# Kernel tuning notes

Measured on AMD Instinct MI355X. Metric: run time of the kernel, lower is better.

Reference implementation:

```python
import jax, jax.numpy as jnp
import numpy as np

B, L, WD, H = 16, 48, 1024, 1024
RANK_H = 128
TEMP = 1.0


def setup_inputs():
    key = jax.random.key(0)
    ks = jax.random.split(key, 10)
    se = jax.random.normal(ks[0], (B, L, WD), jnp.float32)
    length = jnp.clip(jax.random.randint(ks[1], (B,), 8, L + 1), 2, L)
    gumbel_u = jax.random.uniform(ks[2], (B, L), jnp.float32, minval=1e-6, maxval=1.0 - 1e-6)
    sc = 0.02
    Wih = jax.random.normal(ks[3], (4 * H, WD), jnp.float32) * sc
    Whh = jax.random.normal(ks[4], (4 * H, H), jnp.float32) * sc
    bih = jnp.zeros((4 * H,), jnp.float32).at[H:2 * H].set(1.0)  # forget-gate bias = 1
    bhh = jnp.zeros((4 * H,), jnp.float32)
    R1 = jax.random.normal(ks[5], (RANK_H, H), jnp.float32) * 0.01  # rank Linear 1 (no bias)
    R2 = jax.random.normal(ks[6], (1, RANK_H), jnp.float32) * 0.01  # rank Linear 2 (no bias)
    Wc = jax.random.normal(ks[7], (6 * H, 3 * H), jnp.float32) * sc  # Nary compose linear
    bc = jnp.zeros((6 * H,), jnp.float32)
    return dict(sentence_embedding=se, gumbel_u=gumbel_u, Wih=Wih, Whh=Whh,
                bih=bih, bhh=bhh, R1=R1, R2=R2, Wc=Wc, bc=bc, length=length)


def leaf_lstm(x, Wih, Whh, bih, bhh):
    # torch.nn.LSTMCell over time; x: [B, L, WD] -> hs, cs: [B, L, H]
    h0 = jnp.zeros((x.shape[0], H), x.dtype)

    def step(carry, xt):
        h, c = carry
        g = xt @ Wih.T + bih + h @ Whh.T + bhh
        i, f, u, o = jnp.split(g, 4, axis=-1)  # torch gate order i, f, g, o
        c = jax.nn.sigmoid(f) * c + jax.nn.sigmoid(i) * jnp.tanh(u)
        h = jax.nn.sigmoid(o) * jnp.tanh(c)
        return (h, c), (h, c)

    _, (hs, cs) = jax.lax.scan(step, (h0, h0), jnp.swapaxes(x, 0, 1))
    return jnp.swapaxes(hs, 0, 1), jnp.swapaxes(cs, 0, 1)


def nary_cell(lh, lc, rh, rc, xh, xc, Wc, bc):
    # 3-ary tree-LSTM composition: gates i, f_left, f_right, f_x, u, o
    g = jnp.concatenate([lh, rh, xh], axis=-1) @ Wc.T + bc
    i, fl, fr, fx, u, o = jnp.split(g, 6, axis=-1)
    c = (jax.nn.sigmoid(i) * jnp.tanh(u) + jax.nn.sigmoid(fl) * lc
         + jax.nn.sigmoid(fr) * rc + jax.nn.sigmoid(fx) * xc)
    h = jax.nn.sigmoid(o) * jnp.tanh(c)
    return h, c


def build(hs, cs, noise, start, end, R1, R2, Wc, bc):
    # hs, cs: [L, H] for one sentence; returns (h, c) each [H]
    if end <= start:
        z = jnp.zeros((H,), hs.dtype)
        return z, z
    if end == start + 1:
        return hs[start], cs[start]
    x = jax.lax.stop_gradient(hs[start:end])          # rank_detach=True
    s = (jax.nn.relu(x @ R1.T) @ R2.T)[:, 0]          # rank MLP scores [n]
    pos = start + int(jnp.argmax(s))                  # split point = noiseless argmax
    soft = jax.nn.softmax((s + noise[start:end]) / TEMP)
    hard = jax.nn.one_hot(int(jnp.argmax(soft)), end - start, dtype=soft.dtype)
    gate = soft + jax.lax.stop_gradient(hard - soft)  # straight-through gumbel-softmax
    h = gate @ hs[start:end]
    c = gate @ cs[start:end]
    lh, lc = build(hs, cs, noise, start, pos, R1, R2, Wc, bc)
    rh, rc = build(hs, cs, noise, pos + 1, end, R1, R2, Wc, bc)
    return nary_cell(lh, lc, rh, rc, h, c, Wc, bc)


def reference(sentence_embedding, gumbel_u, Wih, Whh, bih, bhh, R1, R2, Wc, bc, length):
    noise = -jnp.log(-jnp.log(gumbel_u))  # Gumbel(0, 1) noise
    hs, cs = leaf_lstm(sentence_embedding, Wih, Whh, bih, bhh)
    lens = [int(v) for v in np.asarray(length)]
    h_res, c_res = [], []
    for b in range(B):
        h, c = build(hs[b], cs[b], noise[b], 0, lens[b], R1, R2, Wc, bc)
        h_res.append(h)
        c_res.append(c)
    return jnp.stack([jnp.stack(h_res), jnp.stack(c_res)])  # [2, B, H]
```

## Files before the change

### kernel.cpp

```cpp
#include <hip/hip_runtime.h>
#include <math.h>

#define BB 16
#define LL 48
#define HH 1024
#define NG4 4096
#define NG6 6144
#define K3H 3072
#define RANKH 128
#define MAXN 47
#define TOTN (BB*MAXN)
#define MAXLVL 48
#define MAXNPL 384

#define FSTRIDE 32
#define FDOM 8192
#define HS_S 1028

typedef __attribute__((ext_vector_type(8))) short bf16x8;
typedef __attribute__((ext_vector_type(4))) float f32x4;

__device__ __forceinline__ float sigf(float x){ return 1.f/(1.f + expf(-x)); }

__device__ __forceinline__ unsigned short f2bf(float f){
  union { float f; unsigned u; } v; v.f = f;
  unsigned r = v.u + 0x7fff + ((v.u >> 16) & 1);
  return (unsigned short)(r >> 16);
}

__device__ __forceinline__ void st_llc(float* p, float v){
  __hip_atomic_store(p, v, __ATOMIC_RELAXED, __HIP_MEMORY_SCOPE_AGENT);
}
__device__ __forceinline__ float ld_llc(const float* p){
  return __hip_atomic_load(p, __ATOMIC_RELAXED, __HIP_MEMORY_SCOPE_AGENT);
}
__device__ __forceinline__ void st_llc_u16(unsigned short* p, unsigned v){
  asm volatile("global_store_short %0, %1, off sc0 sc1" :: "v"(p), "v"(v) : "memory");
}
__device__ __forceinline__ void st_llc_u32(unsigned* p, unsigned v){
  asm volatile("global_store_dword %0, %1, off sc0 sc1" :: "v"(p), "v"(v) : "memory");
}
__device__ __forceinline__ void wait_vm0(){
  asm volatile("s_waitcnt vmcnt(0)" ::: "memory");
}

__device__ __forceinline__ void flagbar(unsigned* flags, unsigned p, int* ldsok){
  wait_vm0();
  __syncthreads();
  int tid = threadIdx.x;
  if (tid == 0)
    st_llc_u32(&flags[blockIdx.x*FSTRIDE], p);
  for (;;){
    unsigned v;
    asm volatile("global_load_dword %0, %1, off sc0 sc1"
                 : "=v"(v) : "v"(&flags[tid*FSTRIDE]));
    wait_vm0();
    int all64 = __all((int)(v >= p));
    if ((tid & 63) == 0) ldsok[tid >> 6] = all64;
    __syncthreads();
    if (ldsok[0] & ldsok[1] & ldsok[2] & ldsok[3]) break;
    __builtin_amdgcn_s_sleep(1);
    __syncthreads();
  }
}

__global__ __launch_bounds__(256) void k_init(unsigned* flags, unsigned short* zrow){
  int tid = threadIdx.x;
  for (int i = tid; i < 2*FDOM; i += 256) flags[i] = 0u;
  for (int i = tid; i < 1024; i += 256) zrow[i] = 0;
}

__global__ __launch_bounds__(256) void k_cvt_bf16(const float* __restrict__ in,
    unsigned short* __restrict__ out, int n){
  int i = (blockIdx.x*256 + threadIdx.x)*4;
  if (i >= n) return;
  float4 v = *(const float4*)(in + i);
  ushort4 o;
  o.x = f2bf(v.x); o.y = f2bf(v.y); o.z = f2bf(v.z); o.w = f2bf(v.w);
  *(ushort4*)(out + i) = o;
}

__global__ __launch_bounds__(256) void k_transpose(const float* __restrict__ in,
                                                   float* __restrict__ out, int R, int C){
  __shared__ float t[32][33];
  int bx = blockIdx.x*32, by = blockIdx.y*32;
  int x = threadIdx.x, y = threadIdx.y;
  #pragma unroll
  for (int i = 0; i < 32; i += 8){
    int r = by + y + i, c = bx + x;
    if (r < R && c < C) t[y+i][x] = in[(size_t)r*C + c];
  }
  __syncthreads();
  #pragma unroll
  for (int i = 0; i < 32; i += 8){
    int r = bx + y + i, c = by + x;
    if (r < C && c < R) out[(size_t)r*R + c] = t[x][y+i];
  }
}

__global__ __launch_bounds__(256) void k_gemm_gx(const float* __restrict__ A,
    const float* __restrict__ Bw, const float* __restrict__ bih,
    const float* __restrict__ bhh, float* __restrict__ Cout, int M, int N, int K){
  __shared__ float as[16][68];
  __shared__ float bs[16][68];
  int m0 = blockIdx.x*64, n0 = blockIdx.y*64;
  int tid = threadIdx.x;
  int mt = tid & 15, nt = tid >> 4;
  float acc[4][4] = {};
  for (int k0 = 0; k0 < K; k0 += 16){
    #pragma unroll
    for (int it = 0; it < 4; ++it){
      int idx = it*256 + tid;
      int kk = idx & 15, mm = idx >> 4;
      as[kk][mm] = A[(size_t)(m0+mm)*K + k0 + kk];
      bs[kk][mm] = Bw[(size_t)(n0+mm)*K + k0 + kk];
    }
    __syncthreads();
    #pragma unroll
    for (int kk = 0; kk < 16; ++kk){
      float a4[4], b4[4];
      #pragma unroll
      for (int i = 0; i < 4; ++i) a4[i] = as[kk][mt*4+i];
      #pragma unroll
      for (int i = 0; i < 4; ++i) b4[i] = bs[kk][nt*4+i];
      #pragma unroll
      for (int i = 0; i < 4; ++i)
        #pragma unroll
        for (int j2 = 0; j2 < 4; ++j2) acc[i][j2] += a4[i]*b4[j2];
    }
    __syncthreads();
  }
  #pragma unroll
  for (int i = 0; i < 4; ++i){
    int m = m0 + mt*4 + i;
    #pragma unroll
    for (int j2 = 0; j2 < 4; ++j2){
      int n = n0 + nt*4 + j2;
      Cout[(size_t)m*N + n] = acc[i][j2] + bih[n] + bhh[n];
    }
  }
}

__global__ __launch_bounds__(256) void k_gx_t(const float* __restrict__ Gx,
                                              float* __restrict__ Gxt){
  __shared__ float t2[16][257];
  int t = blockIdx.x;
  int rc = blockIdx.y;
  int tid = threadIdx.x;
  #pragma unroll
  for (int m = 0; m < 16; ++m)
    t2[m][tid] = Gx[((size_t)(m*48 + t))*4096 + rc*256 + tid];
  __syncthreads();
  int rl = tid >> 4, m = tid & 15;
  #pragma unroll
  for (int i = 0; i < 16; ++i){
    int r = rc*256 + i*16 + rl;
    Gxt[((size_t)t*4096 + r)*16 + m] = t2[m][i*16 + rl];
  }
}

__global__ __launch_bounds__(256, 1) void k_lstm_scan(
    const float* __restrict__ Whh, const float* __restrict__ Gxt,
    float* __restrict__ hx,
    float* __restrict__ hs, float* __restrict__ cs,
    unsigned short* __restrict__ hs_bf, unsigned* __restrict__ flags){
  __shared__ float smem[17408];
  __shared__ float gbuf[4*64];
  __shared__ float cbuf[64];
  __shared__ int ldsok[4];
  int tid = threadIdx.x;
  int g = tid >> 6, kc = tid & 63;
  int j0 = blockIdx.x * 4;
  float w[4][16];
  #pragma unroll
  for (int jj = 0; jj < 4; ++jj){
    const float* src = Whh + (size_t)(g*1024 + j0 + jj)*1024 + kc*4;
    #pragma unroll
    for (int r = 0; r < 4; ++r){
      float4 v = *(const float4*)(src + r*256);
      w[jj][r*4+0]=v.x; w[jj][r*4+1]=v.y; w[jj][r*4+2]=v.z; w[jj][r*4+3]=v.w;
    }
  }
  if (tid < 64) cbuf[tid] = 0.f;
  for (int t = 0; t < LL; ++t){
    float gx = Gxt[((size_t)t*NG4 + g*1024 + j0 + (kc & 3))*16 + (kc >> 2)];
    float G = 0.f;
    if (t > 0){
      const float* slab = hx + (size_t)(t-1)*16384;
      f32x4 hv[16];
      #pragma unroll
      for (int i = 0; i < 16; ++i)
        hv[i] = *(const f32x4*)(slab + i*1024 + tid*4);
      {
        int mb = (tid & 3) * 4;
        int jb = tid >> 2;
        #pragma unroll
        for (int i = 0; i < 16; ++i){
          #pragma unroll
          for (int e = 0; e < 4; ++e)
            smem[(size_t)(mb + e)*HS_S + i*64 + jb] = hv[i][e];
        }
      }
      __syncthreads();
      float acc[4][16];
      #pragma unroll 4
      for (int m = 0; m < 16; ++m){
        const float* hb = &smem[(size_t)m*HS_S + (kc<<2)];
        float4 h0 = *(const float4*)(hb);
        float4 h1 = *(const float4*)(hb+256);
        float4 h2 = *(const float4*)(hb+512);
        float4 h3 = *(const float4*)(hb+768);
        #pragma unroll
        for (int jj = 0; jj < 4; ++jj){
          float s = w[jj][0]*h0.x + w[jj][1]*h0.y + w[jj][2]*h0.z + w[jj][3]*h0.w
                  + w[jj][4]*h1.x + w[jj][5]*h1.y + w[jj][6]*h1.z + w[jj][7]*h1.w
                  + w[jj][8]*h2.x + w[jj][9]*h2.y + w[jj][10]*h2.z + w[jj][11]*h2.w
                  + w[jj][12]*h3.x + w[jj][13]*h3.y + w[jj][14]*h3.z + w[jj][15]*h3.w;
          acc[jj][m] = s;
        }
      }
      __syncthreads();
      #pragma unroll
      for (int m = 0; m < 16; ++m){
        float4 v;
        v.x = acc[0][m]; v.y = acc[1][m]; v.z = acc[2][m]; v.w = acc[3][m];
        *(float4*)&smem[(size_t)(g*64 + kc)*68 + m*4] = v;
      }
      __syncthreads();
      {
        float s0=0.f,s1=0.f,s2=0.f,s3=0.f;
        #pragma unroll 4
        for (int l = 0; l < 64; l += 4){
          s0 += smem[(size_t)(g*64 + l  )*68 + kc];
          s1 += smem[(size_t)(g*64 + l+1)*68 + kc];
          s2 += smem[(size_t)(g*64 + l+2)*68 + kc];
          s3 += smem[(size_t)(g*64 + l+3)*68 + kc];
        }
        G = (s0+s1)+(s2+s3);
      }
    }
    gbuf[g*64 + kc] = G + gx;
    __syncthreads();
    if (g == 0){
      int o = kc;
      int jj = o >> 4, m = o & 15;
      int op = m*4 + jj;
      float gi = gbuf[0*64 + op];
      float gf = gbuf[1*64 + op];
      float gu = gbuf[2*64 + op];
      float go = gbuf[3*64 + op];
      float cp = cbuf[op];
      float c = sigf(gf)*cp + sigf(gi)*tanhf(gu);
      float h = sigf(go)*tanhf(c);
      cbuf[op] = c;
      st_llc(&hx[(size_t)t*16384 + j0*16 + o], h);
      size_t oidx = ((size_t)(m*LL + t))*HH + j0 + jj;
      hs[oidx] = h;
      cs[oidx] = c;
      hs_bf[oidx] = f2bf(h);
    }
    if (t < LL-1)
      flagbar(flags, (unsigned)(t+1), ldsok);
  }
}

__global__ __launch_bounds__(128) void k_score(const float* __restrict__ R1t,
    const float* __restrict__ R2, const float* __restrict__ hs,
    const float* __restrict__ gumbel_u, float* __restrict__ score,
    float* __restrict__ snoisy){
  __shared__ float hsm[HH];
  __shared__ float red[128];
  int bt = blockIdx.x;
  int tid = threadIdx.x;
  for (int i = tid; i < HH; i += 128) hsm[i] = hs[(size_t)bt*HH + i];
  __syncthreads();
  float acc = 0.f;
  for (int k = 0; k < HH; ++k) acc += R1t[(size_t)k*RANKH + tid] * hsm[k];
  red[tid] = fmaxf(acc, 0.f) * R2[tid];
  __syncthreads();
  for (int s = 64; s > 0; s >>= 1){
    if (tid < s) red[tid] += red[tid+s];
    __syncthreads();
  }
  if (tid == 0){
    float s = red[0];
    float u = gumbel_u[bt];
    float noise = -logf(-logf(u));
    score[bt]  = s;
    snoisy[bt] = s + noise;
  }
}

__global__ __launch_bounds__(64) void k_build(const float* __restrict__ score,
    const float* __restrict__ snoisy, const int* __restrict__ length,
    int* __restrict__ node_l, int* __restrict__ node_r, int* __restrict__ node_x,
    int* __restrict__ node_lvl, int* __restrict__ node_b, int* __restrict__ node_root,
    int* __restrict__ level_count, int* __restrict__ level_off, int* __restrict__ order){
  __shared__ float sc[BB*LL], sn[BB*LL];
  __shared__ int lcount[MAXLVL+1], lcur[MAXLVL+1], loff[MAXLVL+1];
  __shared__ int percnt[BB];
  int tid = threadIdx.x;
  for (int i = tid; i < BB*LL; i += 64){ sc[i] = score[i]; sn[i] = snoisy[i]; }
  for (int i = tid; i <= MAXLVL; i += 64){ lcount[i] = 0; lcur[i] = 0; }
  __syncthreads();
  if (tid < BB){
    int b = tid;
    int len = length[b];
    if (len > LL) len = LL;
    int qs[MAXN], qe[MAXN], qn[MAXN];
    int qh = 0, qt = 0, cnt = 0;
    int rootn = cnt++;
    qs[qt] = 0; qe[qt] = len; qn[qt] = rootn; qt++;
    while (qh < qt){
      int s0 = qs[qh], e0 = qe[qh], nid = qn[qh]; qh++;
      float best = sc[b*LL + s0]; int pos = s0;
      for (int t2 = s0+1; t2 < e0; ++t2){
        float v = sc[b*LL + t2];
        if (v > best){ best = v; pos = t2; }
      }
      float bestn = sn[b*LL + s0]; int js = s0;
      for (int t2 = s0+1; t2 < e0; ++t2){
        float v = sn[b*LL + t2];
        if (v > bestn){ bestn = v; js = t2; }
      }
      int gid = b*MAXN + nid;
      node_x[gid] = js;
      node_b[gid] = b;
      node_root[gid] = (nid == 0) ? 1 : 0;
      int ln = pos - s0, enc_l, enc_r;
      if (ln <= 0) enc_l = -1;
      else if (ln == 1) enc_l = 10000 + s0;
      else { int c2 = cnt++; enc_l = b*MAXN + c2; qs[qt]=s0; qe[qt]=pos; qn[qt]=c2; qt++; }
      int rn = e0 - (pos+1);
      if (rn <= 0) enc_r = -1;
      else if (rn == 1) enc_r = 10000 + (pos+1);
      else { int c2 = cnt++; enc_r = b*MAXN + c2; qs[qt]=pos+1; qe[qt]=e0; qn[qt]=c2; qt++; }
      node_l[gid] = enc_l; node_r[gid] = enc_r;
    }
    for (int i = cnt-1; i >= 0; --i){
      int gid = b*MAXN + i;
      int el = node_l[gid], er = node_r[gid];
      int llv = (el >= 0 && el < 10000) ? node_lvl[el] : 0;
      int rlv = (er >= 0 && er < 10000) ? node_lvl[er] : 0;
      node_lvl[gid] = 1 + (llv > rlv ? llv : rlv);
    }
    for (int i = 0; i < cnt; ++i) atomicAdd(&lcount[node_lvl[b*MAXN + i]], 1);
    percnt[b] = cnt;
  }
  __syncthreads();
  if (tid == 0){
    int off = 0, nlev = 0;
    for (int lv = 1; lv <= MAXLVL; ++lv){
      loff[lv] = off;
      level_off[lv] = off;
      level_count[lv] = lcount[lv];
      if (lcount[lv] > 0) nlev = lv;
      off += lcount[lv];
    }
    level_count[0] = nlev;
  }
  __syncthreads();
  if (tid < BB){
    int b = tid;
    int cnt = percnt[b];
    for (int i = 0; i < cnt; ++i){
      int gid = b*MAXN + i;
      int lv = node_lvl[gid];
      int p = atomicAdd(&lcur[lv], 1);
      order[loff[lv] + p] = gid;
    }
  }
}

__global__ __launch_bounds__(256, 1) void k_tree(
    const unsigned short* __restrict__ Wc_bf,
    const unsigned short* __restrict__ hs_bf,
    unsigned short* __restrict__ nodeH_bf,
    const unsigned short* __restrict__ zrow,
    const float* __restrict__ bc, const float* __restrict__ cs,
    float* __restrict__ nodeC,
    const int* __restrict__ node_l, const int* __restrict__ node_r,
    const int* __restrict__ node_x, const int* __restrict__ node_b,
    const int* __restrict__ node_root, const int* __restrict__ level_count,
    const int* __restrict__ level_off, const int* __restrict__ order,
    float* __restrict__ gates, float* __restrict__ out,
    unsigned* __restrict__ flags){
  __shared__ __align__(16) unsigned char wlds[24*6144];
  __shared__ int ldsok[4];
  int tid = threadIdx.x;
  int lane = tid & 63;
  int wave = tid >> 6;
  int fr = lane & 15;
  int fkq = lane >> 4;
  int fk  = fkq * 8;
  int fkb = fkq * 16;
  int swz = (fr & 7) << 4;
  int base0 = fr * 6144;
  int base1 = (16 + (fr & 7)) * 6144;
  int rg24 = blockIdx.x * 24;

  for (int i = tid; i < 24*384; i += 256){
    int row = i / 384;
    int ch  = i - row*384;
    uint4 v = *(const uint4*)(Wc_bf + (size_t)(rg24 + row)*K3H + ch*8);
    *(uint4*)(wlds + row*6144 + ((ch*16) ^ ((row & 7) << 4))) = v;
  }
  __syncthreads();

  int nlev = level_count[0];
  unsigned ph = 0;
  for (int lvl = 1; lvl <= nlev; ++lvl){
    int n = level_count[lvl];
    int loffv = level_off[lvl];
    int mtiles = (n + 15) >> 4;
    for (int mt = wave; mt < mtiles; mt += 4){
      int slot = mt*16 + fr;
      const unsigned short *pa0, *pa1, *pa2;
      if (slot < n){
        int gid = order[loffv + slot];
        int b = node_b[gid];
        int el = node_l[gid], er = node_r[gid], xt = node_x[gid];
        pa0 = (el < 0) ? zrow : (el >= 10000 ? hs_bf + (size_t)(b*LL + (el-10000))*HH
                                             : nodeH_bf + (size_t)el*HH);
        pa1 = (er < 0) ? zrow : (er >= 10000 ? hs_bf + (size_t)(b*LL + (er-10000))*HH
                                             : nodeH_bf + (size_t)er*HH);
        pa2 = hs_bf + (size_t)(b*LL + xt)*HH;
      } else { pa0 = zrow; pa1 = zrow; pa2 = zrow; }
      const unsigned short* pa[3] = {pa0, pa1, pa2};
      f32x4 acc0 = {0.f,0.f,0.f,0.f};
      f32x4 acc1 = {0.f,0.f,0.f,0.f};
      #pragma unroll
      for (int part = 0; part < 3; ++part){
        const unsigned short* ap = pa[part] + fk;
        #pragma unroll 8
        for (int kcc = 0; kcc < 1024; kcc += 32){
          bf16x8 a = *(const bf16x8*)(ap + kcc);
          int xb = part*2048 + kcc*2 + fkb;
          bf16x8 b0 = *(const bf16x8*)(wlds + base0 + (xb ^ swz));
          bf16x8 b1 = *(const bf16x8*)(wlds + base1 + (xb ^ swz));
          acc0 = __builtin_amdgcn_mfma_f32_16x16x32_bf16(a, b0, acc0, 0, 0, 0);
          acc1 = __builtin_amdgcn_mfma_f32_16x16x32_bf16(a, b1, acc1, 0, 0, 0);
        }
      }
      int m0 = mt*16 + fkq*4;
      #pragma unroll
      for (int r = 0; r < 4; ++r){
        int m = m0 + r;
        if (m < n){
          st_llc(&gates[(size_t)m*NG6 + rg24 + fr], acc0[r]);
          if (fr < 8)
            st_llc(&gates[(size_t)m*NG6 + rg24 + 16 + fr], acc1[r]);
        }
      }
    }
    ph++;
    flagbar(flags, ph, ldsok);
    int items = n * 4;
    for (int it = blockIdx.x; it < items; it += 256){
      int ns = it >> 2;
      int j = (it & 3)*256 + tid;
      int gid = order[loffv + ns];
      int b = node_b[gid];
      int el = node_l[gid], er = node_r[gid], xt = node_x[gid];
      float gg[6];
      #pragma unroll
      for (int q = 0; q < 6; ++q)
        gg[q] = bc[q*HH + j] + ld_llc(&gates[(size_t)ns*NG6 + q*HH + j]);
      float lc = (el < 0) ? 0.f : (el >= 10000 ? cs[(size_t)(b*LL + (el-10000))*HH + j]
                                               : nodeC[(size_t)el*HH + j]);
      float rc = (er < 0) ? 0.f : (er >= 10000 ? cs[(size_t)(b*LL + (er-10000))*HH + j]
                                               : nodeC[(size_t)er*HH + j]);
      float xc = cs[(size_t)(b*LL + xt)*HH + j];
      float c = sigf(gg[0])*tanhf(gg[4]) + sigf(gg[1])*lc + sigf(gg[2])*rc + sigf(gg[3])*xc;
      float h = sigf(gg[5])*tanhf(c);
      st_llc_u16(&nodeH_bf[(size_t)gid*HH + j], (unsigned)f2bf(h));
      st_llc(&nodeC[(size_t)gid*HH + j], c);
      if (node_root[gid]){
        out[(size_t)b*HH + j] = h;
        out[(size_t)BB*HH + (size_t)b*HH + j] = c;
      }
    }
    if (lvl < nlev){
      ph++;
      flagbar(flags, ph, ldsok);
    }
  }
}

extern "C" void kernel_launch(void* const* d_in, const int* in_sizes, int n_in,
                              void* d_out, int out_size, void* d_ws, size_t ws_size,
                              hipStream_t stream){
  const float* se  = (const float*)d_in[0];
  const float* gu  = (const float*)d_in[1];
  const float* Wih = (const float*)d_in[2];
  const float* Whh = (const float*)d_in[3];
  const float* bih = (const float*)d_in[4];
  const float* bhh = (const float*)d_in[5];
  const float* R1  = (const float*)d_in[6];
  const float* R2  = (const float*)d_in[7];
  const float* Wc  = (const float*)d_in[8];
  const float* bc  = (const float*)d_in[9];
  const int*   len = (const int*)d_in[10];
  float* out = (float*)d_out;

  float* ws = (float*)d_ws;
  size_t off = 0;
  float* R1t   = ws + off; off += (size_t)HH*RANKH;
  float* Gx    = ws + off; off += (size_t)BB*LL*NG4;
  float* Gxt   = ws + off; off += (size_t)BB*LL*NG4;
  float* hx    = ws + off; off += (size_t)LL*HH*BB;
  float* hs    = ws + off; off += (size_t)BB*LL*HH;
  float* cs    = ws + off; off += (size_t)BB*LL*HH;
  float* nodeC = ws + off; off += (size_t)TOTN*HH;
  float* gates = ws + off; off += (size_t)MAXNPL*NG6;
  unsigned short* Wc_bf    = (unsigned short*)(ws + off); off += (size_t)NG6*K3H/2;
  unsigned short* hs_bf    = (unsigned short*)(ws + off); off += (size_t)BB*LL*HH/2;
  unsigned short* nodeH_bf = (unsigned short*)(ws + off); off += (size_t)TOTN*HH/2 + 512;
  unsigned short* zrow     = (unsigned short*)(ws + off); off += 512;
  float* score = ws + off; off += 1024;
  float* snoi  = ws + off; off += 1024;
  unsigned* flags = (unsigned*)(ws + off); off += 2*FDOM;
  int* ib = (int*)(ws + off);
  int* node_l    = ib; ib += 768;
  int* node_r    = ib; ib += 768;
  int* node_x    = ib; ib += 768;
  int* node_lvl  = ib; ib += 768;
  int* node_b    = ib; ib += 768;
  int* node_root = ib; ib += 768;
  int* level_count = ib; ib += 64;
  int* level_off   = ib; ib += 64;
  int* order       = ib; ib += 768;

  k_init<<<1, 256, 0, stream>>>(flags, zrow);
  k_transpose<<<dim3(32, 4), dim3(32, 8), 0, stream>>>(R1, R1t, RANKH, HH);
  k_cvt_bf16<<<(NG6*K3H)/1024, 256, 0, stream>>>(Wc, Wc_bf, NG6*K3H);
  k_gemm_gx<<<dim3(12, 64), 256, 0, stream>>>(se, Wih, bih, bhh, Gx, BB*LL, NG4, HH);
  k_gx_t<<<dim3(48, 16), 256, 0, stream>>>(Gx, Gxt);
  k_lstm_scan<<<256, 256, 0, stream>>>(Whh, Gxt, hx, hs, cs, hs_bf, flags);
  k_score<<<BB*LL, 128, 0, stream>>>(R1t, R2, hs, gu, score, snoi);
  k_build<<<1, 64, 0, stream>>>(score, snoi, len, node_l, node_r, node_x,
                                node_lvl, node_b, node_root,
                                level_count, level_off, order);
  k_tree<<<256, 256, 0, stream>>>(Wc_bf, hs_bf, nodeH_bf, zrow, bc, cs, nodeC,
                                  node_l, node_r, node_x, node_b, node_root,
                                  level_count, level_off, order,
                                  gates, out, flags + FDOM);
}
```

Before: 1.055 ms.

## Compute input projection GEMM with split-bf16 MFMA instead of FP32 SIMT

Replaces the FP32 shared-memory tiled GEMM for the LSTM input projection with a matrix-core kernel. Inputs and Wih are split into bf16 hi/lo pairs and combined with three MFMA products to keep near-FP32 accuracy. The split buffers are placed temporarily in the Wc_bf workspace, so the Wc conversion kernel is moved after the GEMM. This adds two split kernels and extra memory traffic while reducing GEMM compute time.

Result: no change. 1.073 ms (+1.7%).

```diff
diff --git a/kernel.cpp b/kernel.cpp
--- a/kernel.cpp
+++ b/kernel.cpp
@@ -26,6 +26,10 @@
   union { float f; unsigned u; } v; v.f = f;
   unsigned r = v.u + 0x7fff + ((v.u >> 16) & 1);
   return (unsigned short)(r >> 16);
+}
+__device__ __forceinline__ float bf2f(unsigned short h){
+  union { unsigned u; float f; } v; v.u = ((unsigned)h) << 16;
+  return v.f;
 }
 
 __device__ __forceinline__ void st_llc(float* p, float v){
@@ -80,6 +84,19 @@
   *(ushort4*)(out + i) = o;
 }
 
+__global__ __launch_bounds__(256) void k_split(const float* __restrict__ in,
+    unsigned short* __restrict__ hi, unsigned short* __restrict__ lo, int n){
+  int i = (blockIdx.x*256 + threadIdx.x)*4;
+  if (i >= n) return;
+  float4 v = *(const float4*)(in + i);
+  ushort4 h, l;
+  h.x = f2bf(v.x); h.y = f2bf(v.y); h.z = f2bf(v.z); h.w = f2bf(v.w);
+  l.x = f2bf(v.x - bf2f(h.x)); l.y = f2bf(v.y - bf2f(h.y));
+  l.z = f2bf(v.z - bf2f(h.z)); l.w = f2bf(v.w - bf2f(h.w));
+  *(ushort4*)(hi + i) = h;
+  *(ushort4*)(lo + i) = l;
+}
+
 __global__ __launch_bounds__(256) void k_transpose(const float* __restrict__ in,
                                                    float* __restrict__ out, int R, int C){
   __shared__ float t[32][33];
@@ -98,47 +115,42 @@
   }
 }
 
-__global__ __launch_bounds__(256) void k_gemm_gx(const float* __restrict__ A,
-    const float* __restrict__ Bw, const float* __restrict__ bih,
-    const float* __restrict__ bhh, float* __restrict__ Cout, int M, int N, int K){
-  __shared__ float as[16][68];
-  __shared__ float bs[16][68];
-  int m0 = blockIdx.x*64, n0 = blockIdx.y*64;
-  int tid = threadIdx.x;
-  int mt = tid & 15, nt = tid >> 4;
-  float acc[4][4] = {};
-  for (int k0 = 0; k0 < K; k0 += 16){
+__global__ __launch_bounds__(256) void k_gemm_gx_mfma(
+    const unsigned short* __restrict__ Ah, const unsigned short* __restrict__ Al,
+    const unsigned short* __restrict__ Bh, const unsigned short* __restrict__ Bl,
+    const float* __restrict__ bih, const float* __restrict__ bhh,
+    float* __restrict__ Gx){
+  int tid = threadIdx.x;
+  int lane = tid & 63, wave = tid >> 6;
+  int fr = lane & 15, fkq = lane >> 4, fk = fkq*8;
+  int m0 = blockIdx.x*64 + wave*16;
+  int n0 = blockIdx.y*64;
+  const unsigned short* ah = Ah + (size_t)(m0 + fr)*1024 + fk;
+  const unsigned short* al = Al + (size_t)(m0 + fr)*1024 + fk;
+  const unsigned short* bh0 = Bh + (size_t)(n0 + fr)*1024 + fk;
+  const unsigned short* bl0 = Bl + (size_t)(n0 + fr)*1024 + fk;
+  f32x4 acc[4] = {{0.f,0.f,0.f,0.f},{0.f,0.f,0.f,0.f},
+                  {0.f,0.f,0.f,0.f},{0.f,0.f,0.f,0.f}};
+  for (int kc = 0; kc < 1024; kc += 32){
+    bf16x8 a1 = *(const bf16x8*)(ah + kc);
+    bf16x8 a2 = *(const bf16x8*)(al + kc);
     #pragma unroll
-    for (int it = 0; it < 4; ++it){
-      int idx = it*256 + tid;
-      int kk = idx & 15, mm = idx >> 4;
-      as[kk][mm] = A[(size_t)(m0+mm)*K + k0 + kk];
-      bs[kk][mm] = Bw[(size_t)(n0+mm)*K + k0 + kk];
-    }
-    __syncthreads();
+    for (int ng = 0; ng < 4; ++ng){
+      bf16x8 b1 = *(const bf16x8*)(bh0 + (size_t)ng*16*1024 + kc);
+      bf16x8 b2 = *(const bf16x8*)(bl0 + (size_t)ng*16*1024 + kc);
+      acc[ng] = __builtin_amdgcn_mfma_f32_16x16x32_bf16(a1, b1, acc[ng], 0, 0, 0);
+      acc[ng] = __builtin_amdgcn_mfma_f32_16x16x32_bf16(a2, b1, acc[ng], 0, 0, 0);
+      acc[ng] = __builtin_amdgcn_mfma_f32_16x16x32_bf16(a1, b2, acc[ng], 0, 0, 0);
+    }
+  }
+  #pragma unroll
+  for (int ng = 0; ng < 4; ++ng)
     #pragma unroll
-    for (int kk = 0; kk < 16; ++kk){
-      float a4[4], b4[4];
-      #pragma unroll
-      for (int i = 0; i < 4; ++i) a4[i] = as[kk][mt*4+i];
-      #pragma unroll
-      for (int i = 0; i < 4; ++i) b4[i] = bs[kk][nt*4+i];
-      #pragma unroll
-      for (int i = 0; i < 4; ++i)
-        #pragma unroll
-        for (int j2 = 0; j2 < 4; ++j2) acc[i][j2] += a4[i]*b4[j2];
-    }
-    __syncthreads();
-  }
-  #pragma unroll
-  for (int i = 0; i < 4; ++i){
-    int m = m0 + mt*4 + i;
-    #pragma unroll
-    for (int j2 = 0; j2 < 4; ++j2){
-      int n = n0 + nt*4 + j2;
-      Cout[(size_t)m*N + n] = acc[i][j2] + bih[n] + bhh[n];
-    }
-  }
+    for (int r = 0; r < 4; ++r){
+      int m = m0 + fkq*4 + r;
+      int n = n0 + ng*16 + fr;
+      Gx[(size_t)m*NG4 + n] = acc[ng][r] + bih[n] + bhh[n];
+    }
 }
 
 __global__ __launch_bounds__(256) void k_gx_t(const float* __restrict__ Gx,
@@ -531,11 +543,19 @@
   int* level_off   = ib; ib += 64;
   int* order       = ib; ib += 768;
 
+  unsigned short* seh   = Wc_bf;
+  unsigned short* sel   = Wc_bf + 786432;
+  unsigned short* wih_h = Wc_bf + 2*786432;
+  unsigned short* wih_l = Wc_bf + 2*786432 + 4194304;
+
   k_init<<<1, 256, 0, stream>>>(flags, zrow);
   k_transpose<<<dim3(32, 4), dim3(32, 8), 0, stream>>>(R1, R1t, RANKH, HH);
+  k_split<<<768, 256, 0, stream>>>(se, seh, sel, 786432);
+  k_split<<<4096, 256, 0, stream>>>(Wih, wih_h, wih_l, 4194304);
+  k_gemm_gx_mfma<<<dim3(12, 64), 256, 0, stream>>>(seh, sel, wih_h, wih_l,
+                                                   bih, bhh, Gx);
+  k_gx_t<<<dim3(48, 16), 256, 0, stream>>>(Gx, Gxt);
   k_cvt_bf16<<<(NG6*K3H)/1024, 256, 0, stream>>>(Wc, Wc_bf, NG6*K3H);
-  k_gemm_gx<<<dim3(12, 64), 256, 0, stream>>>(se, Wih, bih, bhh, Gx, BB*LL, NG4, HH);
-  k_gx_t<<<dim3(48, 16), 256, 0, stream>>>(Gx, Gxt);
   k_lstm_scan<<<256, 256, 0, stream>>>(Whh, Gxt, hx, hs, cs, hs_bf, flags);
   k_score<<<BB*LL, 128, 0, stream>>>(R1t, R2, hs, gu, score, snoi);
   k_build<<<1, 64, 0, stream>>>(score, snoi, len, node_l, node_r, node_x,
```
